# Performance work log

Measured on AMD Instinct MI355X. Metric: run time of the kernel, lower is better.

Reference implementation:

```python
import jax, jax.numpy as jnp
import numpy as np

# Constants from UpFIRDn2dJIT(channel=64, lrelu_upsampling=2, filter_size=6, kernel_size=3)
# with init_kernel(in_size=128, out_size=128): up_factor = dn_factor = 2.
UP = 2
DN = 2
SLOPE = 0.2
GAIN = 1.4142135623730951  # sqrt(2)
CROP = 1  # kernel_size - 1 - kernel_size//2 for kernel_size=3
IN_SIZE = 128
FILTER_SIZE = 6
B, C = 8, 64


def _firwin_lowpass(numtaps, cutoff, width, fs):
    # Reproduces scipy.signal.firwin(numtaps, cutoff, width=width, fs=fs)
    # (lowpass, pass_zero=True, scale=True, Kaiser window from `width`).
    nyq = 0.5 * fs
    atten = 2.285 * (numtaps - 1) * np.pi * (width / nyq) + 7.95  # kaiser_atten
    if atten > 50:
        beta = 0.1102 * (atten - 8.7)
    elif atten > 21:
        beta = 0.5842 * (atten - 21) ** 0.4 + 0.07886 * (atten - 21)
    else:
        beta = 0.0
    m = np.arange(numtaps) - (numtaps - 1) / 2.0
    c = cutoff / nyq
    h = c * np.sinc(c * m) * np.kaiser(numtaps, beta)
    h = h / h.sum()  # scale so DC gain == 1
    return h.astype(np.float32)


def _conv1d_same(x, f, axis):
    # x: [N, 1, H, W]; 1D cross-correlation along `axis` (2 or 3) with torch
    # padding='same' semantics for even taps: left pad = (K-1)//2, right pad gets the extra.
    K = f.shape[0]
    pl = (K - 1) // 2
    pr = (K - 1) - pl
    if axis == 2:
        kern = f.reshape(1, 1, K, 1)
        pad = [(pl, pr), (0, 0)]
    else:
        kern = f.reshape(1, 1, 1, K)
        pad = [(0, 0), (pl, pr)]
    return jax.lax.conv_general_dilated(
        x, kern, window_strides=(1, 1), padding=pad,
        dimension_numbers=("NCHW", "OIHW", "NCHW"))


def _forward(x, bias, up_filter, dn_filter):
    x = x[:, :, CROP:-CROP, CROP:-CROP]            # [B, C, 128, 128]
    b, c, h, w = x.shape
    x = x + bias[None, :, None, None]
    x = x.reshape(b * c, 1, h, w)
    x = jnp.repeat(jnp.repeat(x, UP, axis=2), UP, axis=3)
    # outer(f, f) conv == separable 1D convs (filter is an outer product)
    x = _conv1d_same(_conv1d_same(x, up_filter, 2), up_filter, 3)
    x = jnp.where(x >= 0, x, SLOPE * x) * GAIN     # leaky ReLU * gain
    x = _conv1d_same(_conv1d_same(x, dn_filter, 2), dn_filter, 3)
    x = x[:, :, ::DN, ::DN]                        # grid_pool2d -> [B*C, 1, 128, 128]
    return x.reshape(b, c, x.shape[2], x.shape[3])


def setup_inputs() -> dict:
    key = jax.random.key(0)
    kx, = jax.random.split(key, 1)
    x = jax.random.normal(kx, (B, C, IN_SIZE + 2 * CROP, IN_SIZE + 2 * CROP), dtype=jnp.float32)
    bias = jnp.zeros((C,), dtype=jnp.float32)  # nn.Parameter init to zeros
    taps = FILTER_SIZE * UP  # 12
    up_filter = jnp.asarray(_firwin_lowpass(taps, IN_SIZE / 2.0001, IN_SIZE, IN_SIZE))
    dn_filter = jnp.asarray(_firwin_lowpass(taps, IN_SIZE / 2.0001, IN_SIZE, IN_SIZE))
    return {"x": x, "bias": bias, "up_filter": up_filter, "dn_filter": dn_filter}


def reference(x, bias, up_filter, dn_filter):
    return _forward(x, bias, up_filter, dn_filter)
```

## Files before the change

kernel.cpp:

```cpp
#include <hip/hip_runtime.h>


#define GAIN_C 1.4142135623730951f
#define NEG2_C (0.2f - 1.0f)

typedef short v8s __attribute__((ext_vector_type(8)));
typedef float v4f __attribute__((ext_vector_type(4)));
typedef float f4u __attribute__((ext_vector_type(4), aligned(4)));

__device__ __forceinline__ void pinv(v8s& x) { asm volatile("" : "+v"(x)); }

__device__ __forceinline__ int f2bf(float f) {
    unsigned u = __float_as_uint(f);
    return (int)((u + 0x7FFFu + ((u >> 16) & 1u)) >> 16) & 0xFFFF;
}
__device__ __forceinline__ int pack_bf2(float a, float b) {
#if __has_builtin(__builtin_amdgcn_cvt_pk_bf16_f32)
    typedef __bf16 bf2 __attribute__((ext_vector_type(2)));
    bf2 r = __builtin_amdgcn_cvt_pk_bf16_f32(a, b);
    int o; __builtin_memcpy(&o, &r, 4); return o;
#else
    return f2bf(a) | (f2bf(b) << 16);
#endif
}

__device__ float band(int x, int q, int qlim, int xlim, const float* fu) {
    if (q >= qlim || x >= xlim || x < 0) return 0.f;
    int p = q >> 1, d = x - p;
    if (q & 1) {
        if (d < 0 || d > 6) return 0.f;
        if (d == 0) return fu[0];
        if (d == 6) return fu[11];
        return fu[2 * d - 1] + fu[2 * d];
    } else {
        if (d < 0 || d > 5) return 0.f;
        return fu[2 * d] + fu[2 * d + 1];
    }
}
__device__ float dband(int o, int q, int v, int qlim, const float* fd) {
    if (q >= qlim || q < 0) return 0.f;
    if (v == 0 && q < 5) return 0.f;
    if (v == 2 && q >= qlim - 5) return 0.f;
    int k = q - 2 * o;
    if (k < 0 || k > 11) return 0.f;
    return fd[k];
}

__global__ __launch_bounds__(256) void build_consts(
    const float* __restrict__ fu, const float* __restrict__ fd,
    short* __restrict__ ws)
{
    int idx = blockIdx.x * 256 + threadIdx.x;
    int l = (idx >> 3) & 63, j = idx & 7;
    int l15 = l & 15, kq = (l >> 4) * 8 + j;
    float val;
    if (idx < 2560) {
        int nt = idx >> 9;
        int k0 = 8 * nt < 16 ? 8 * nt : 16;
        val = band(k0 + kq, 16 * nt + l15, 74, 43, fu);
    } else if (idx < 7168) {
        int mt = (idx - 2560) >> 9;
        int k0 = 8 * mt < 48 ? 8 * mt : 48;
        val = band(k0 + kq, 16 * mt + l15, 138, 75, fu);
    } else if (idx < 15360) {
        int rel = idx - 7168;
        int v = (rel >> 12) ? 2 : 0;
        int fi = (rel & 4095) >> 9;
        int mt = fi >> 1, kt = fi & 1;
        int k0 = 32 * mt < 80 ? 32 * mt : 80;
        val = dband(16 * mt + l15, k0 + 32 * kt + kq, v, 138, fd) * GAIN_C;
    } else {
        int rel = idx - 15360;
        int v = rel >> 11, fi = (rel & 2047) >> 9;
        int nt = fi >> 1, kt = fi & 1;
        int k0 = nt ? 16 : 0;
        val = dband(16 * nt + l15, k0 + 32 * kt + kq, v, 74, fd);
    }
    ws[idx] = (short)f2bf(val);
}

#define XPITCH 48
#define BPITCH 88
#define UPITCH 152
#define TPITCH 88

template<int BASE, int N>
__device__ __forceinline__ void s1_window(
    const short* __restrict__ GtB, const short* __restrict__ Xl,
    short* __restrict__ B1t, int lane, int l15, int q4)
{
    v8s bf[N], a[N];
#pragma unroll
    for (int i = 0; i < N; ++i) {
        const int t = BASE + i;
        const int nt = t - (t / 5) * 5;
        bf[i] = *(const v8s*)&GtB[nt * 512 + lane * 8];
    }
#pragma unroll
    for (int i = 0; i < N; ++i) {
        const int t = BASE + i;
        const int mt = t / 5, nt = t - mt * 5;
        const int k0 = 8 * nt < 16 ? 8 * nt : 16;
        a[i] = *(const v8s*)&Xl[(16 * mt + l15) * XPITCH + k0 + q4 * 8];
    }
#pragma unroll
    for (int i = 0; i < N; ++i) { pinv(bf[i]); pinv(a[i]); }
#pragma unroll
    for (int i = 0; i < N; ++i) {
        const int t = BASE + i;
        const int mt = t / 5, nt = t - mt * 5;
        v4f acc = {0.f, 0.f, 0.f, 0.f};
        acc = __builtin_amdgcn_mfma_f32_16x16x32_bf16(a[i], bf[i], acc, 0, 0, 0);
        *(int2*)&B1t[(16 * nt + l15) * BPITCH + 16 * mt + q4 * 4] =
            make_int2(pack_bf2(acc[0], acc[1]), pack_bf2(acc[2], acc[3]));
    }
}

template<int BASE, int N>
__device__ __forceinline__ void s2_window(
    const short* __restrict__ G2A, const short* __restrict__ B1t,
    short* __restrict__ Ut, int lane, int l15, int q4)
{
    constexpr int MT0 = BASE / 5;
    constexpr int MTL = (BASE + N - 1) / 5;
    v8s af0, af1{};
    af0 = *(const v8s*)&G2A[MT0 * 512 + lane * 8];
    if constexpr (MTL != MT0)
        af1 = *(const v8s*)&G2A[MTL * 512 + lane * 8];
    v8s b[N];
#pragma unroll
    for (int i = 0; i < N; ++i) {
        const int t = BASE + i;
        const int mt = t / 5, nt = t - mt * 5;
        const int k0 = 8 * mt < 48 ? 8 * mt : 48;
        b[i] = *(const v8s*)&B1t[(16 * nt + l15) * BPITCH + k0 + q4 * 8];
    }
    pinv(af0);
    if constexpr (MTL != MT0) pinv(af1);
#pragma unroll
    for (int i = 0; i < N; ++i) pinv(b[i]);
#pragma unroll
    for (int i = 0; i < N; ++i) {
        const int t = BASE + i;
        const int mt = t / 5, nt = t - mt * 5;
        const v8s af = (mt == MT0) ? af0 : af1;
        v4f acc = {0.f, 0.f, 0.f, 0.f};
        acc = __builtin_amdgcn_mfma_f32_16x16x32_bf16(af, b[i], acc, 0, 0, 0);
#pragma unroll
        for (int j = 0; j < 4; ++j)
            acc[j] = acc[j] + NEG2_C * fminf(acc[j], 0.f);
        *(int2*)&Ut[(16 * nt + l15) * UPITCH + 16 * mt + q4 * 4] =
            make_int2(pack_bf2(acc[0], acc[1]), pack_bf2(acc[2], acc[3]));
    }
}

template<int BASE, int N>
__device__ __forceinline__ void s3_window(
    const short* __restrict__ DA, const short* __restrict__ Ut,
    short* __restrict__ T, int lane, int l15, int q4)
{
    constexpr int MT0 = BASE / 5;
    constexpr int MTL = (BASE + N - 1) / 5;
    v8s a00, a01, a10{}, a11{};
    a00 = *(const v8s*)&DA[(MT0 * 2 + 0) * 512 + lane * 8];
    a01 = *(const v8s*)&DA[(MT0 * 2 + 1) * 512 + lane * 8];
    if constexpr (MTL != MT0) {
        a10 = *(const v8s*)&DA[(MTL * 2 + 0) * 512 + lane * 8];
        a11 = *(const v8s*)&DA[(MTL * 2 + 1) * 512 + lane * 8];
    }
    v8s b0[N], b1[N];
#pragma unroll
    for (int i = 0; i < N; ++i) {
        const int t = BASE + i;
        const int mt = t / 5, nt = t - mt * 5;
        const int k0 = 32 * mt < 80 ? 32 * mt : 80;
        b0[i] = *(const v8s*)&Ut[(16 * nt + l15) * UPITCH + k0 + q4 * 8];
        b1[i] = *(const v8s*)&Ut[(16 * nt + l15) * UPITCH + k0 + 32 + q4 * 8];
    }
    pinv(a00); pinv(a01);
    if constexpr (MTL != MT0) { pinv(a10); pinv(a11); }
#pragma unroll
    for (int i = 0; i < N; ++i) { pinv(b0[i]); pinv(b1[i]); }
#pragma unroll
    for (int i = 0; i < N; ++i) {
        const int t = BASE + i;
        const int mt = t / 5, nt = t - mt * 5;
        const v8s a0 = (mt == MT0) ? a00 : a10;
        const v8s a1 = (mt == MT0) ? a01 : a11;
        v4f acc = {0.f, 0.f, 0.f, 0.f};
        acc = __builtin_amdgcn_mfma_f32_16x16x32_bf16(a0, b0[i], acc, 0, 0, 0);
        acc = __builtin_amdgcn_mfma_f32_16x16x32_bf16(a1, b1[i], acc, 0, 0, 0);
        int p01 = pack_bf2(acc[0], acc[1]);
        int p23 = pack_bf2(acc[2], acc[3]);
        short* tb = &T[(16 * mt + q4 * 4) * TPITCH + 16 * nt + l15];
        tb[0 * TPITCH] = (short)p01;
        tb[1 * TPITCH] = (short)(p01 >> 16);
        tb[2 * TPITCH] = (short)p23;
        tb[3 * TPITCH] = (short)(p23 >> 16);
    }
}

template<int W>
__device__ __forceinline__ void s1_phase(
    const short* __restrict__ GtB, const short* __restrict__ Xl,
    short* __restrict__ B1t, int lane, int l15, int q4)
{
    if constexpr (W == 0) s1_window<0, 4>(GtB, Xl, B1t, lane, l15, q4);
    else                  s1_window<3 * W + 1, 3>(GtB, Xl, B1t, lane, l15, q4);
}

template<int W>
__device__ __forceinline__ void s2_phase(
    const short* __restrict__ G2A, const short* __restrict__ B1t,
    short* __restrict__ Ut, int lane, int l15, int q4)
{
    if constexpr (W < 5) s2_window<6 * W, 6>(G2A, B1t, Ut, lane, l15, q4);
    else                 s2_window<5 * W + 5, 5>(G2A, B1t, Ut, lane, l15, q4);
}

template<int W>
__device__ __forceinline__ void s3_phase(
    const short* __restrict__ DA, const short* __restrict__ Ut,
    short* __restrict__ T, int lane, int l15, int q4)
{
    if constexpr (W < 4) s3_window<3 * W, 3>(DA, Ut, T, lane, l15, q4);
    else                 s3_window<2 * W + 4, 2>(DA, Ut, T, lane, l15, q4);
}

template<int W>
__device__ __forceinline__ void s4_phase(
    const short* __restrict__ T, const short* __restrict__ D2B,
    float* __restrict__ out, size_t obase_c, int i0, int j0, int l15, int q4,
    int lane)
{
    constexpr int mt = W >> 1, nt = W & 1;
    constexpr int k0 = nt ? 16 : 0;
    v8s b0 = *(const v8s*)&D2B[(nt * 2 + 0) * 512 + lane * 8];
    v8s b1 = *(const v8s*)&D2B[(nt * 2 + 1) * 512 + lane * 8];
    v8s a0 = *(const v8s*)&T[(16 * mt + l15) * TPITCH + k0 + q4 * 8];
    v8s a1 = *(const v8s*)&T[(16 * mt + l15) * TPITCH + k0 + 32 + q4 * 8];
    pinv(b0); pinv(b1); pinv(a0); pinv(a1);
    v4f acc = {0.f, 0.f, 0.f, 0.f};
    acc = __builtin_amdgcn_mfma_f32_16x16x32_bf16(a0, b0, acc, 0, 0, 0);
    acc = __builtin_amdgcn_mfma_f32_16x16x32_bf16(a1, b1, acc, 0, 0, 0);
    float* op = out + obase_c
              + (size_t)(i0 + 16 * mt + q4 * 4) * 128 + (j0 + 16 * nt + l15);
#pragma unroll
    for (int i = 0; i < 4; ++i) op[i * 128] = acc[i];
}

#define DISP8(CALL)                                                          \
    if      (w == 0) { CALL(0) } else if (w == 1) { CALL(1) }                \
    else if (w == 2) { CALL(2) } else if (w == 3) { CALL(3) }                \
    else if (w == 4) { CALL(4) } else if (w == 5) { CALL(5) }                \
    else if (w == 6) { CALL(6) } else { CALL(7) }

__global__ __launch_bounds__(512, 6) void upfirdn_mfma(
    const float* __restrict__ xin_all,
    const float* __restrict__ bias,
    const short* __restrict__ cws,
    float* __restrict__ out)
{
    __shared__ __align__(16) short SH[19200];
    short* B1t = SH;
    short* Ut  = SH + 7040;
    short* Xl  = SH + 7040;
    short* T   = SH;

    const int tid  = threadIdx.x;
    const int lane = tid & 63, w = tid >> 6;
    const int l15  = lane & 15, q4 = lane >> 4;
    const int bx = blockIdx.x, by = blockIdx.y, bc = blockIdx.z;
    const int i0 = by * 64, j0 = bx * 32;

    const short* GtB = cws;
    const short* G2A = cws + 2560;
    const short* DA  = cws + 7168  + (by ? 4096 : 0);
    const short* D2B = cws + 15360 + ((bx == 0) ? 0 : (bx == 3) ? 2 : 1) * 2048;

    if (tid < 480) {
        const int r  = tid / 6, c6 = tid - 6 * r;
        const int gr = i0 - 5 + r;
        int* dst = (int*)Xl + r * 24 + 4 * c6;
        if (r < 75 && (unsigned)gr < 128u) {
            const float* rowp = xin_all + (size_t)bc * (130 * 130)
                              + (gr + 1) * 130 + (j0 - 4) + 8 * c6;
            f4u v0 = *(const f4u*)rowp;
            f4u v1 = *(const f4u*)(rowp + 4);
            const float bv = bias[bc & 63];
            const bool colInt = (bx == 1) | (bx == 2);
            float f[8];
#pragma unroll
            for (int j = 0; j < 8; ++j) {
                const int c = 8 * c6 + j;
                bool valid = c < 43;
                if (!colInt) valid = valid && ((unsigned)(j0 - 5 + c) < 128u);
                const float xv = (j < 4) ? v0[j] : v1[j - 4];
                f[j] = valid ? xv + bv : 0.f;
            }
            *(int4*)dst = make_int4(pack_bf2(f[0], f[1]), pack_bf2(f[2], f[3]),
                                    pack_bf2(f[4], f[5]), pack_bf2(f[6], f[7]));
        } else {
            *(int4*)dst = make_int4(0, 0, 0, 0);
        }
    }
    __syncthreads();

#define S1C(W) s1_phase<W>(GtB, Xl, B1t, lane, l15, q4);
    DISP8(S1C)
#undef S1C
    __syncthreads();

#define S2C(W) s2_phase<W>(G2A, B1t, Ut, lane, l15, q4);
    DISP8(S2C)
#undef S2C
    __syncthreads();

#define S3C(W) s3_phase<W>(DA, Ut, T, lane, l15, q4);
    DISP8(S3C)
#undef S3C
    __syncthreads();

    const size_t obase_c = (size_t)bc * 16384;
#define S4C(W) s4_phase<W>(T, D2B, out, obase_c, i0, j0, l15, q4, lane);
    DISP8(S4C)
#undef S4C
}

extern "C" void kernel_launch(void* const* d_in, const int* in_sizes, int n_in,
                              void* d_out, int out_size, void* d_ws, size_t ws_size,
                              hipStream_t stream) {
    const float* x  = (const float*)d_in[0];
    const float* bs = (const float*)d_in[1];
    const float* fu = (const float*)d_in[2];
    const float* fd = (const float*)d_in[3];
    float* outp = (float*)d_out;
    short* ws = (short*)d_ws;

    build_consts<<<84, 256, 0, stream>>>(fu, fd, ws);
    upfirdn_mfma<<<dim3(4, 2, 512), 512, 0, stream>>>(x, bs, ws, outp);
}
```

Measured before the change: 108.0 us.

## Fuse stages 3 and 4 in registers using transposed MFMA and 16x16x16 chaining

Merges the vertical downsample (stage 3) and horizontal downsample (stage 4) into one per-wave phase. Stage 3 now computes a transposed tile whose accumulator layout feeds directly as the A operand of a 16x16x16 bf16 MFMA against a repacked D2B constant. This drops the LDS round trip through T and one __syncthreads. The cost is redundant stage-3 work, since each wave recomputes five tiles per output tile, and a different constant layout that needs more build_consts blocks.

New measurement: 113.3 us. 4.9% more time.

```diff
diff --git a/kernel.cpp b/kernel.cpp
--- a/kernel.cpp
+++ b/kernel.cpp
@@ -5,10 +5,25 @@
 #define NEG2_C (0.2f - 1.0f)
 
 typedef short v8s __attribute__((ext_vector_type(8)));
+typedef short v4s __attribute__((ext_vector_type(4)));
 typedef float v4f __attribute__((ext_vector_type(4)));
 typedef float f4u __attribute__((ext_vector_type(4), aligned(4)));
 
 __device__ __forceinline__ void pinv(v8s& x) { asm volatile("" : "+v"(x)); }
+__device__ __forceinline__ void pinv4(v4s& x) { asm volatile("" : "+v"(x)); }
+
+__device__ __forceinline__ v4f mfma16(v4s a, v4s b, v4f c) {
+#if __has_builtin(__builtin_amdgcn_mfma_f32_16x16x16_bf16)
+    return __builtin_amdgcn_mfma_f32_16x16x16_bf16(a, b, c, 0, 0, 0);
+#elif __has_builtin(__builtin_amdgcn_mfma_f32_16x16x16bf16_1k)
+    return __builtin_amdgcn_mfma_f32_16x16x16bf16_1k(a, b, c, 0, 0, 0);
+#else
+    v4f d;
+    asm volatile("v_mfma_f32_16x16x16_bf16 %0, %1, %2, %3"
+                 : "=v"(d) : "v"(a), "v"(b), "v"(c));
+    return d;
+#endif
+}
 
 __device__ __forceinline__ int f2bf(float f) {
     unsigned u = __float_as_uint(f);
@@ -51,30 +66,35 @@
     short* __restrict__ ws)
 {
     int idx = blockIdx.x * 256 + threadIdx.x;
-    int l = (idx >> 3) & 63, j = idx & 7;
-    int l15 = l & 15, kq = (l >> 4) * 8 + j;
     float val;
-    if (idx < 2560) {
-        int nt = idx >> 9;
-        int k0 = 8 * nt < 16 ? 8 * nt : 16;
-        val = band(k0 + kq, 16 * nt + l15, 74, 43, fu);
-    } else if (idx < 7168) {
-        int mt = (idx - 2560) >> 9;
-        int k0 = 8 * mt < 48 ? 8 * mt : 48;
-        val = band(k0 + kq, 16 * mt + l15, 138, 75, fu);
-    } else if (idx < 15360) {
-        int rel = idx - 7168;
-        int v = (rel >> 12) ? 2 : 0;
-        int fi = (rel & 4095) >> 9;
-        int mt = fi >> 1, kt = fi & 1;
-        int k0 = 32 * mt < 80 ? 32 * mt : 80;
-        val = dband(16 * mt + l15, k0 + 32 * kt + kq, v, 138, fd) * GAIN_C;
+    if (idx < 15360) {
+        int l = (idx >> 3) & 63, j = idx & 7;
+        int l15 = l & 15, kq = (l >> 4) * 8 + j;
+        if (idx < 2560) {
+            int nt = idx >> 9;
+            int k0 = 8 * nt < 16 ? 8 * nt : 16;
+            val = band(k0 + kq, 16 * nt + l15, 74, 43, fu);
+        } else if (idx < 7168) {
+            int mt = (idx - 2560) >> 9;
+            int k0 = 8 * mt < 48 ? 8 * mt : 48;
+            val = band(k0 + kq, 16 * mt + l15, 138, 75, fu);
+        } else {
+            int rel = idx - 7168;
+            int v = (rel >> 12) ? 2 : 0;
+            int fi = (rel & 4095) >> 9;
+            int amt = fi >> 1, kt = fi & 1;
+            int k0 = 32 * amt < 80 ? 32 * amt : 80;
+            val = dband(16 * amt + l15, k0 + 32 * kt + kq, v, 138, fd) * GAIN_C;
+        }
     } else {
         int rel = idx - 15360;
-        int v = rel >> 11, fi = (rel & 2047) >> 9;
-        int nt = fi >> 1, kt = fi & 1;
-        int k0 = nt ? 16 : 0;
-        val = dband(16 * nt + l15, k0 + 32 * kt + kq, v, 74, fd);
+        int v = rel / 2560, r2 = rel - v * 2560;
+        int frag = r2 >> 8;
+        int nt = frag >> 1, jt = frag & 1;
+        int lane = (r2 & 255) >> 2, jj = r2 & 3;
+        int o = 16 * jt + (lane & 15);
+        int q = 16 * nt + (lane >> 4) * 4 + jj;
+        val = dband(o, q, v, 74, fd);
     }
     ws[idx] = (short)f2bf(val);
 }
@@ -82,7 +102,6 @@
 #define XPITCH 48
 #define BPITCH 88
 #define UPITCH 152
-#define TPITCH 88
 
 template<int BASE, int N>
 __device__ __forceinline__ void s1_window(
@@ -154,50 +173,45 @@
     }
 }
 
-template<int BASE, int N>
-__device__ __forceinline__ void s3_window(
-    const short* __restrict__ DA, const short* __restrict__ Ut,
-    short* __restrict__ T, int lane, int l15, int q4)
-{
-    constexpr int MT0 = BASE / 5;
-    constexpr int MTL = (BASE + N - 1) / 5;
-    v8s a00, a01, a10{}, a11{};
-    a00 = *(const v8s*)&DA[(MT0 * 2 + 0) * 512 + lane * 8];
-    a01 = *(const v8s*)&DA[(MT0 * 2 + 1) * 512 + lane * 8];
-    if constexpr (MTL != MT0) {
-        a10 = *(const v8s*)&DA[(MTL * 2 + 0) * 512 + lane * 8];
-        a11 = *(const v8s*)&DA[(MTL * 2 + 1) * 512 + lane * 8];
-    }
-    v8s b0[N], b1[N];
-#pragma unroll
-    for (int i = 0; i < N; ++i) {
-        const int t = BASE + i;
-        const int mt = t / 5, nt = t - mt * 5;
-        const int k0 = 32 * mt < 80 ? 32 * mt : 80;
-        b0[i] = *(const v8s*)&Ut[(16 * nt + l15) * UPITCH + k0 + q4 * 8];
-        b1[i] = *(const v8s*)&Ut[(16 * nt + l15) * UPITCH + k0 + 32 + q4 * 8];
-    }
-    pinv(a00); pinv(a01);
-    if constexpr (MTL != MT0) { pinv(a10); pinv(a11); }
-#pragma unroll
-    for (int i = 0; i < N; ++i) { pinv(b0[i]); pinv(b1[i]); }
-#pragma unroll
-    for (int i = 0; i < N; ++i) {
-        const int t = BASE + i;
-        const int mt = t / 5, nt = t - mt * 5;
-        const v8s a0 = (mt == MT0) ? a00 : a10;
-        const v8s a1 = (mt == MT0) ? a01 : a11;
-        v4f acc = {0.f, 0.f, 0.f, 0.f};
-        acc = __builtin_amdgcn_mfma_f32_16x16x32_bf16(a0, b0[i], acc, 0, 0, 0);
-        acc = __builtin_amdgcn_mfma_f32_16x16x32_bf16(a1, b1[i], acc, 0, 0, 0);
-        int p01 = pack_bf2(acc[0], acc[1]);
-        int p23 = pack_bf2(acc[2], acc[3]);
-        short* tb = &T[(16 * mt + q4 * 4) * TPITCH + 16 * nt + l15];
-        tb[0 * TPITCH] = (short)p01;
-        tb[1 * TPITCH] = (short)(p01 >> 16);
-        tb[2 * TPITCH] = (short)p23;
-        tb[3 * TPITCH] = (short)(p23 >> 16);
-    }
+template<int W>
+__device__ __forceinline__ void s34_phase(
+    const short* __restrict__ DA, const short* __restrict__ D2B,
+    const short* __restrict__ Ut, float* __restrict__ out,
+    size_t obase_c, int i0, int j0, int lane, int l15, int q4)
+{
+    constexpr int amt = W >> 1, jt = W & 1;
+    constexpr int k0 = 32 * amt < 80 ? 32 * amt : 80;
+    v8s bp0 = *(const v8s*)&DA[(amt * 2 + 0) * 512 + lane * 8];
+    v8s bp1 = *(const v8s*)&DA[(amt * 2 + 1) * 512 + lane * 8];
+    v4s d2[5];
+#pragma unroll
+    for (int nt = 0; nt < 5; ++nt)
+        d2[nt] = *(const v4s*)&D2B[(nt * 2 + jt) * 256 + lane * 4];
+    v8s ut0[5], ut1[5];
+#pragma unroll
+    for (int nt = 0; nt < 5; ++nt) {
+        ut0[nt] = *(const v8s*)&Ut[(16 * nt + l15) * UPITCH + k0 + q4 * 8];
+        ut1[nt] = *(const v8s*)&Ut[(16 * nt + l15) * UPITCH + k0 + 32 + q4 * 8];
+    }
+    pinv(bp0); pinv(bp1);
+#pragma unroll
+    for (int nt = 0; nt < 5; ++nt) { pinv4(d2[nt]); pinv(ut0[nt]); pinv(ut1[nt]); }
+
+    v4f accO = {0.f, 0.f, 0.f, 0.f};
+#pragma unroll
+    for (int nt = 0; nt < 5; ++nt) {
+        v4f t = {0.f, 0.f, 0.f, 0.f};
+        t = __builtin_amdgcn_mfma_f32_16x16x32_bf16(ut0[nt], bp0, t, 0, 0, 0);
+        t = __builtin_amdgcn_mfma_f32_16x16x32_bf16(ut1[nt], bp1, t, 0, 0, 0);
+        union { int i2[2]; v4s s; } a16;
+        a16.i2[0] = pack_bf2(t[0], t[1]);
+        a16.i2[1] = pack_bf2(t[2], t[3]);
+        accO = mfma16(a16.s, d2[nt], accO);
+    }
+    float* op = out + obase_c
+              + (size_t)(i0 + 16 * amt + q4 * 4) * 128 + (j0 + 16 * jt + l15);
+#pragma unroll
+    for (int i = 0; i < 4; ++i) op[i * 128] = accO[i];
 }
 
 template<int W>
@@ -216,37 +230,6 @@
 {
     if constexpr (W < 5) s2_window<6 * W, 6>(G2A, B1t, Ut, lane, l15, q4);
     else                 s2_window<5 * W + 5, 5>(G2A, B1t, Ut, lane, l15, q4);
-}
-
-template<int W>
-__device__ __forceinline__ void s3_phase(
-    const short* __restrict__ DA, const short* __restrict__ Ut,
-    short* __restrict__ T, int lane, int l15, int q4)
-{
-    if constexpr (W < 4) s3_window<3 * W, 3>(DA, Ut, T, lane, l15, q4);
-    else                 s3_window<2 * W + 4, 2>(DA, Ut, T, lane, l15, q4);
-}
-
-template<int W>
-__device__ __forceinline__ void s4_phase(
-    const short* __restrict__ T, const short* __restrict__ D2B,
-    float* __restrict__ out, size_t obase_c, int i0, int j0, int l15, int q4,
-    int lane)
-{
-    constexpr int mt = W >> 1, nt = W & 1;
-    constexpr int k0 = nt ? 16 : 0;
-    v8s b0 = *(const v8s*)&D2B[(nt * 2 + 0) * 512 + lane * 8];
-    v8s b1 = *(const v8s*)&D2B[(nt * 2 + 1) * 512 + lane * 8];
-    v8s a0 = *(const v8s*)&T[(16 * mt + l15) * TPITCH + k0 + q4 * 8];
-    v8s a1 = *(const v8s*)&T[(16 * mt + l15) * TPITCH + k0 + 32 + q4 * 8];
-    pinv(b0); pinv(b1); pinv(a0); pinv(a1);
-    v4f acc = {0.f, 0.f, 0.f, 0.f};
-    acc = __builtin_amdgcn_mfma_f32_16x16x32_bf16(a0, b0, acc, 0, 0, 0);
-    acc = __builtin_amdgcn_mfma_f32_16x16x32_bf16(a1, b1, acc, 0, 0, 0);
-    float* op = out + obase_c
-              + (size_t)(i0 + 16 * mt + q4 * 4) * 128 + (j0 + 16 * nt + l15);
-#pragma unroll
-    for (int i = 0; i < 4; ++i) op[i * 128] = acc[i];
 }
 
 #define DISP8(CALL)                                                          \
@@ -265,7 +248,6 @@
     short* B1t = SH;
     short* Ut  = SH + 7040;
     short* Xl  = SH + 7040;
-    short* T   = SH;
 
     const int tid  = threadIdx.x;
     const int lane = tid & 63, w = tid >> 6;
@@ -276,7 +258,7 @@
     const short* GtB = cws;
     const short* G2A = cws + 2560;
     const short* DA  = cws + 7168  + (by ? 4096 : 0);
-    const short* D2B = cws + 15360 + ((bx == 0) ? 0 : (bx == 3) ? 2 : 1) * 2048;
+    const short* D2B = cws + 15360 + ((bx == 0) ? 0 : (bx == 3) ? 2 : 1) * 2560;
 
     if (tid < 480) {
         const int r  = tid / 6, c6 = tid - 6 * r;
@@ -316,15 +298,10 @@
 #undef S2C
     __syncthreads();
 
-#define S3C(W) s3_phase<W>(DA, Ut, T, lane, l15, q4);
-    DISP8(S3C)
-#undef S3C
-    __syncthreads();
-
     const size_t obase_c = (size_t)bc * 16384;
-#define S4C(W) s4_phase<W>(T, D2B, out, obase_c, i0, j0, l15, q4, lane);
-    DISP8(S4C)
-#undef S4C
+#define S34C(W) s34_phase<W>(DA, D2B, Ut, out, obase_c, i0, j0, lane, l15, q4);
+    DISP8(S34C)
+#undef S34C
 }
 
 extern "C" void kernel_launch(void* const* d_in, const int* in_sizes, int n_in,
@@ -337,6 +314,6 @@
     float* outp = (float*)d_out;
     short* ws = (short*)d_ws;
 
-    build_consts<<<84, 256, 0, stream>>>(fu, fd, ws);
+    build_consts<<<90, 256, 0, stream>>>(fu, fd, ws);
     upfirdn_mfma<<<dim3(4, 2, 512), 512, 0, stream>>>(x, bs, ws, outp);
 }
```
